# Performance work log

Hardware: AMD Instinct MI355X
Metric: run time of the kernel (lower is better)

Reference implementation:

```python
import jax, jax.numpy as jnp
import numpy as np

N = 100000   # nodes
E = 800000   # edges (avg degree ~8)
G = 64       # graphs in batch
F_IN = 64
H = 128
C = 4


def setup_inputs() -> dict:
    key = jax.random.key(0)
    ks = jax.random.split(key, 14)
    def w(k, fin, fout):
        return jax.random.normal(k, (fin, fout), dtype=jnp.float32) * (1.0 / np.sqrt(fin))
    inp = {
        "x": jax.random.normal(ks[0], (N, F_IN), dtype=jnp.float32),
        "W1": w(ks[1], F_IN, H), "b1": jnp.zeros((H,), jnp.float32),
        "W2": w(ks[2], H, H),    "b2": jnp.zeros((H,), jnp.float32),
        "W3": w(ks[3], H, H),    "b3": jnp.zeros((H,), jnp.float32),
        "fw1": w(ks[4], H, H),   "fb1": jnp.zeros((H,), jnp.float32),
        "fw2": w(ks[5], H, C),   "fb2": jnp.zeros((C,), jnp.float32),
        "edge_index": jax.random.randint(ks[6], (2, E), 0, N, dtype=jnp.int32),
        "batch": jnp.sort(jax.random.randint(ks[7], (N,), 0, G, dtype=jnp.int32)),
    }
    return inp


def gcn_conv(x, W, b, src, dst):
    """PyG GCNConv: linear transform, add self-loops, symmetric deg^-1/2 norm, scatter-add."""
    h = x @ W                                                    # [N, H]
    deg = jax.ops.segment_sum(jnp.ones((E,), x.dtype), dst, num_segments=N) + 1.0  # self-loop
    dinv = jax.lax.rsqrt(deg)                                    # [N]
    norm = dinv[src] * dinv[dst]                                 # [E]
    agg = jax.ops.segment_sum(h[src] * norm[:, None], dst, num_segments=N)
    agg = agg + h * (dinv * dinv)[:, None]                       # self-loop term (norm = 1/deg)
    return agg + b


def reference(x, W1, b1, W2, b2, W3, b3, fw1, fb1, fw2, fb2, edge_index, batch):
    src, dst = edge_index[0], edge_index[1]
    h = jax.nn.relu(gcn_conv(x, W1, b1, src, dst))
    h = jax.nn.relu(gcn_conv(h, W2, b2, src, dst))
    h = gcn_conv(h, W3, b3, src, dst)
    # global mean pool over graphs
    s = jax.ops.segment_sum(h, batch, num_segments=G)            # [G, H]
    cnt = jax.ops.segment_sum(jnp.ones((N,), h.dtype), batch, num_segments=G)
    pooled = s / jnp.maximum(cnt, 1.0)[:, None]
    z = jax.nn.relu(pooled @ fw1 + fb1)
    return z @ fw2 + fb2                                          # [G, C]
```

## Files before the change

### kernel.cpp

```cpp
#include <hip/hip_runtime.h>

#define N_NODES 100000
#define N_EDGES 800000
#define G_GRAPHS 64
#define F_INPUT 64
#define H_DIM 128
#define C_OUT 4
#define CSR_CAP 32
#define EDGE_BLOCKS (N_EDGES / 256)
#define CONV_BLOCKS ((N_NODES + 255) / 256)
#define WPACK_BLOCKS 20
#define FILL_SEG 4
#define FILL_CHUNKS 250
#define FILL_RANGE (N_NODES / FILL_SEG)
#define FILL_CHUNK (N_EDGES / FILL_CHUNKS)
#define FILL_BLOCKS (FILL_SEG * FILL_CHUNKS)
#define SEG_SPAN (FILL_RANGE * CSR_CAP)

typedef __attribute__((ext_vector_type(8))) short bf16x8;
typedef __attribute__((ext_vector_type(8))) unsigned short u16x8;
typedef __attribute__((ext_vector_type(4))) float f32x4;

__device__ inline unsigned short f2bf(float f) {
    union { float f; unsigned int u; } v; v.f = f;
    unsigned int u = v.u + 0x7FFFu + ((v.u >> 16) & 1u);
    return (unsigned short)(u >> 16);
}
__device__ inline float bf2f(unsigned short b) {
    union { unsigned int u; float f; } v; v.u = ((unsigned int)b) << 16;
    return v.f;
}
__device__ inline float2 unpack_pair(unsigned int u) {
    union { unsigned int u; float f; } a, b;
    a.u = u << 16; b.u = u & 0xFFFF0000u;
    float2 r; r.x = a.f; r.y = b.f; return r;
}
__device__ inline unsigned char f2fp8(float v) {
    int r = __builtin_amdgcn_cvt_pk_fp8_f32(v, 0.0f, 0, false);
    return (unsigned char)(r & 0xFF);
}

__device__ inline void wpack_one(const float* __restrict__ W, unsigned short* __restrict__ hi,
                                 unsigned short* __restrict__ lo, int K, int t)
{
    int lane = t & 63;
    int tile = t >> 6;
    int KS = K / 32;
    int ct = tile / KS, ks = tile % KS;
    int n  = ct * 16 + (lane & 15);
    int k0 = ks * 32 + (lane >> 4) * 8;
    #pragma unroll
    for (int j = 0; j < 8; j++) {
        float w = W[(k0 + j) * H_DIM + n];
        unsigned short h = f2bf(w);
        hi[t * 8 + j] = h;
        lo[t * 8 + j] = f2bf(w - bf2f(h));
    }
}

__global__ __launch_bounds__(256) void hist_kernel(
    const int* __restrict__ dst, int* __restrict__ cnt, int* __restrict__ paddr,
    const float* __restrict__ W1, const float* __restrict__ W2, const float* __restrict__ W3,
    unsigned short* __restrict__ w1hi, unsigned short* __restrict__ w1lo,
    unsigned short* __restrict__ w2hi, unsigned short* __restrict__ w2lo,
    unsigned short* __restrict__ w3hi, unsigned short* __restrict__ w3lo)
{
    int b = blockIdx.x;
    if (b < EDGE_BLOCKS) {
        int e = b * 256 + threadIdx.x;
        int d = dst[e];
        int sl = atomicAdd(&cnt[d], 1);
        paddr[e] = (sl < CSR_CAP) ? d * CSR_CAP + sl : -1;
        return;
    }
    b -= EDGE_BLOCKS;
    int t = b * 256 + threadIdx.x;
    if (t < 1024)       wpack_one(W1, w1hi, w1lo, F_INPUT, t);
    else if (t < 3072)  wpack_one(W2, w2hi, w2lo, H_DIM, t - 1024);
    else                wpack_one(W3, w3hi, w3lo, H_DIM, t - 3072);
}

__global__ __launch_bounds__(256) void prep_kernel(
    const int* __restrict__ paddr, const int* __restrict__ src,
    int* __restrict__ csr,
    const int* __restrict__ cnti, const float4* __restrict__ x4,
    float* __restrict__ dinv, unsigned int* __restrict__ xb_u,
    unsigned int* __restrict__ p1z, unsigned int* __restrict__ p3z)
{
    int b = blockIdx.x;
    if (b < FILL_BLOCKS) {
        const int r   = b & (FILL_SEG - 1);
        const int m   = b >> 2;
        const int plo = r * SEG_SPAN;
        const int phi = plo + SEG_SPAN;
        const int e0  = m * FILL_CHUNK;
        for (int e = e0 + threadIdx.x; e < e0 + FILL_CHUNK; e += 256) {
            int pa = paddr[e];
            if (pa >= plo && pa < phi)
                csr[pa] = src[e];
        }
        return;
    }
    b -= FILL_BLOCKS;
    __shared__ float dl[256];
    int i = b * 256 + threadIdx.x;
    float dv = 0.0f;
    if (i < N_NODES) {
        int c  = cnti[i];
        int dc = min(c, CSR_CAP);
        dv = rsqrtf((float)c + 1.0f);
        dinv[i] = dv;
        int pad = (dc + 7) & ~7;
        for (int s2 = dc; s2 < pad; s2++)
            csr[(size_t)i * CSR_CAP + s2] = N_NODES;
    } else if (i == N_NODES) {
        for (int c = 0; c < 32; c++) {
            xb_u[(size_t)N_NODES * 32 + c] = 0u;
            p1z [(size_t)N_NODES * 32 + c] = 0u;
            p3z [(size_t)N_NODES * 32 + c] = 0u;
        }
    }
    dl[threadIdx.x] = dv;
    __syncthreads();
    const int row_base = b * 256;
    for (int c = threadIdx.x; c < 256 * 16; c += 256) {
        int r = c >> 4;
        int row = row_base + r;
        if (row < N_NODES) {
            float d2 = dl[r];
            float4 v = x4[(size_t)row * 16 + (c & 15)];
            size_t o = ((size_t)row * 16 + (c & 15)) * 2;
            xb_u[o + 0] = (unsigned int)f2bf(v.x * d2) | ((unsigned int)f2bf(v.y * d2) << 16);
            xb_u[o + 1] = (unsigned int)f2bf(v.z * d2) | ((unsigned int)f2bf(v.w * d2) << 16);
        }
    }
}

__global__ __launch_bounds__(256) void gemm_g1f_kernel(
    const uint2* __restrict__ xb2, const int* __restrict__ cnti,
    const int* __restrict__ csr, const float* __restrict__ dinv,
    const unsigned short* __restrict__ whi, const unsigned short* __restrict__ wlo,
    const float* __restrict__ bias, unsigned char* __restrict__ out8)
{
    constexpr int KS = 2;
    __shared__ unsigned short As[16 * 64];
    uint2* As2 = (uint2*)As;
    const int tid  = threadIdx.x;
    const int row0 = blockIdx.x * 16;

    {
        int r  = tid >> 4;
        int f8 = tid & 15;
        int gr = row0 + r;
        int dc = min(cnti[gr], CSR_CAP);
        int beg  = gr * CSR_CAP;
        int end8 = beg + ((dc + 7) & ~7);
        const uint2* base = xb2 + f8;
        float a0, a1, a2, a3;
        {
            uint2 w = base[(size_t)gr * 16];
            float2 p0 = unpack_pair(w.x), p1 = unpack_pair(w.y);
            a0 = p0.x; a1 = p0.y; a2 = p1.x; a3 = p1.y;
        }
        for (int e = beg; e < end8; e += 8) {
            int4 c0 = *(const int4*)(csr + e);
            int4 c1 = *(const int4*)(csr + e + 4);
            uint2 w0 = base[(size_t)c0.x * 16];
            uint2 w1 = base[(size_t)c0.y * 16];
            uint2 w2 = base[(size_t)c0.z * 16];
            uint2 w3 = base[(size_t)c0.w * 16];
            uint2 w4 = base[(size_t)c1.x * 16];
            uint2 w5 = base[(size_t)c1.y * 16];
            uint2 w6 = base[(size_t)c1.z * 16];
            uint2 w7 = base[(size_t)c1.w * 16];
            #pragma unroll
            for (uint2 w : {w0, w1, w2, w3, w4, w5, w6, w7}) {
                float2 p0 = unpack_pair(w.x), p1 = unpack_pair(w.y);
                a0 += p0.x; a1 += p0.y; a2 += p1.x; a3 += p1.y;
            }
        }
        float dv = dinv[gr];
        uint2 o;
        o.x = (unsigned int)f2bf(a0 * dv) | ((unsigned int)f2bf(a1 * dv) << 16);
        o.y = (unsigned int)f2bf(a2 * dv) | ((unsigned int)f2bf(a3 * dv) << 16);
        int ks = f8 >> 3, quad = (f8 >> 1) & 3, bb = f8 & 1;
        As2[((ks * 64 + quad * 16 + r) << 1) | bb] = o;
    }
    __syncthreads();

    const int w = tid >> 6, lane = tid & 63;
    const int quad = lane >> 4, l16 = lane & 15;
    const int ct0 = w * 2;

    f32x4 acc[2];
    acc[0] = (f32x4)(0.0f);
    acc[1] = (f32x4)(0.0f);
    #pragma unroll
    for (int ks = 0; ks < KS; ks++) {
        bf16x8 a0 = *(const bf16x8*)(As + (ks * 64 + lane) * 8);
        bf16x8 bh[2], bl[2];
        #pragma unroll
        for (int c = 0; c < 2; c++) {
            bh[c] = *(const bf16x8*)(whi + ((size_t)((ct0 + c) * KS + ks) * 64 + lane) * 8);
            bl[c] = *(const bf16x8*)(wlo + ((size_t)((ct0 + c) * KS + ks) * 64 + lane) * 8);
        }
        #pragma unroll
        for (int c = 0; c < 2; c++) {
            acc[c] = __builtin_amdgcn_mfma_f32_16x16x32_bf16(a0, bh[c], acc[c], 0, 0, 0);
            acc[c] = __builtin_amdgcn_mfma_f32_16x16x32_bf16(a0, bl[c], acc[c], 0, 0, 0);
        }
    }
    float bv[2];
    #pragma unroll
    for (int c = 0; c < 2; c++) bv[c] = bias[(ct0 + c) * 16 + l16];
    #pragma unroll
    for (int reg = 0; reg < 4; reg++) {
        int row = row0 + quad * 4 + reg;
        #pragma unroll
        for (int c = 0; c < 2; c++) {
            float val = fmaxf(acc[c][reg] + bv[c], 0.0f);
            out8[(size_t)row * H_DIM + (ct0 + c) * 16 + l16] = f2fp8(val);
        }
    }
}

__device__ inline void acc_u2(uint2 w, float* __restrict__ a) {
    auto l0 = __builtin_amdgcn_cvt_pk_f32_fp8(w.x, false);
    auto h0 = __builtin_amdgcn_cvt_pk_f32_fp8(w.x, true);
    auto l1 = __builtin_amdgcn_cvt_pk_f32_fp8(w.y, false);
    auto h1 = __builtin_amdgcn_cvt_pk_f32_fp8(w.y, true);
    a[0] += l0[0]; a[1] += l0[1]; a[2] += h0[0]; a[3] += h0[1];
    a[4] += l1[0]; a[5] += l1[1]; a[6] += h1[0]; a[7] += h1[1];
}
__device__ inline void gather_fp8_u2(
    const uint2* __restrict__ base, const int* __restrict__ csr,
    int i, int beg, int end8, float* __restrict__ a)
{
    acc_u2(base[(size_t)i * 16], a);
    for (int e = beg; e < end8; e += 8) {
        int4 c0 = *(const int4*)(csr + e);
        int4 c1 = *(const int4*)(csr + e + 4);
        uint2 w0 = base[(size_t)c0.x * 16];
        uint2 w1 = base[(size_t)c0.y * 16];
        uint2 w2 = base[(size_t)c0.z * 16];
        uint2 w3 = base[(size_t)c0.w * 16];
        uint2 w4 = base[(size_t)c1.x * 16];
        uint2 w5 = base[(size_t)c1.y * 16];
        uint2 w6 = base[(size_t)c1.z * 16];
        uint2 w7 = base[(size_t)c1.w * 16];
        acc_u2(w0, a); acc_u2(w1, a); acc_u2(w2, a); acc_u2(w3, a);
        acc_u2(w4, a); acc_u2(w5, a); acc_u2(w6, a); acc_u2(w7, a);
    }
}

__global__ __launch_bounds__(256) void gemm_g2f_kernel(
    const uint2* __restrict__ hs8, const int* __restrict__ cnti,
    const int* __restrict__ csr, const float* __restrict__ dinv,
    const unsigned short* __restrict__ whi, const unsigned short* __restrict__ wlo,
    const float* __restrict__ bias, unsigned char* __restrict__ out8)
{
    constexpr int KS = 4;
    __shared__ unsigned short As[16 * 128];
    uint4* As4 = (uint4*)As;
    const int tid  = threadIdx.x;
    const int row0 = blockIdx.x * 16;

    {
        int r  = tid >> 4;
        int f8 = tid & 15;
        int gr = row0 + r;
        int dc = min(cnti[gr], CSR_CAP);
        int beg  = gr * CSR_CAP;
        int end8 = beg + ((dc + 7) & ~7);
        float a[8] = {0, 0, 0, 0, 0, 0, 0, 0};
        gather_fp8_u2(hs8 + f8, csr, gr, beg, end8, a);
        float dv = dinv[gr];
        float4 b0 = *(const float4*)(bias + f8 * 8);
        float4 b1 = *(const float4*)(bias + f8 * 8 + 4);
        float v0 = fmaxf(a[0] * dv + b0.x, 0.0f);
        float v1 = fmaxf(a[1] * dv + b0.y, 0.0f);
        float v2 = fmaxf(a[2] * dv + b0.z, 0.0f);
        float v3 = fmaxf(a[3] * dv + b0.w, 0.0f);
        float v4 = fmaxf(a[4] * dv + b1.x, 0.0f);
        float v5 = fmaxf(a[5] * dv + b1.y, 0.0f);
        float v6 = fmaxf(a[6] * dv + b1.z, 0.0f);
        float v7 = fmaxf(a[7] * dv + b1.w, 0.0f);
        uint4 o;
        o.x = (unsigned int)f2bf(v0) | ((unsigned int)f2bf(v1) << 16);
        o.y = (unsigned int)f2bf(v2) | ((unsigned int)f2bf(v3) << 16);
        o.z = (unsigned int)f2bf(v4) | ((unsigned int)f2bf(v5) << 16);
        o.w = (unsigned int)f2bf(v6) | ((unsigned int)f2bf(v7) << 16);
        As4[(f8 >> 2) * 64 + (f8 & 3) * 16 + r] = o;
    }
    __syncthreads();

    const int w = tid >> 6, lane = tid & 63;
    const int quad = lane >> 4, l16 = lane & 15;
    const int ct0 = w * 2;

    f32x4 acc[2];
    acc[0] = (f32x4)(0.0f);
    acc[1] = (f32x4)(0.0f);
    #pragma unroll
    for (int ks = 0; ks < KS; ks++) {
        bf16x8 a0 = *(const bf16x8*)(As + (ks * 64 + lane) * 8);
        bf16x8 bh[2], bl[2];
        #pragma unroll
        for (int c = 0; c < 2; c++) {
            bh[c] = *(const bf16x8*)(whi + ((size_t)((ct0 + c) * KS + ks) * 64 + lane) * 8);
            bl[c] = *(const bf16x8*)(wlo + ((size_t)((ct0 + c) * KS + ks) * 64 + lane) * 8);
        }
        #pragma unroll
        for (int c = 0; c < 2; c++) {
            acc[c] = __builtin_amdgcn_mfma_f32_16x16x32_bf16(a0, bh[c], acc[c], 0, 0, 0);
            acc[c] = __builtin_amdgcn_mfma_f32_16x16x32_bf16(a0, bl[c], acc[c], 0, 0, 0);
        }
    }
    #pragma unroll
    for (int reg = 0; reg < 4; reg++) {
        int row = row0 + quad * 4 + reg;
        float dvr = dinv[row];
        #pragma unroll
        for (int c = 0; c < 2; c++)
            out8[(size_t)row * H_DIM + (ct0 + c) * 16 + l16] = f2fp8(acc[c][reg] * dvr);
    }
}

__global__ __launch_bounds__(256) void gather3_kernel(
    const uint2* __restrict__ hs8, const int* __restrict__ cnti,
    const int* __restrict__ csr, const float* __restrict__ dinv,
    const float* __restrict__ bias, uint4* __restrict__ outb)
{
    int idx = blockIdx.x * 256 + threadIdx.x;
    int i  = idx >> 4;
    int f8 = idx & 15;
    int dc = min(cnti[i], CSR_CAP);
    int beg  = i * CSR_CAP;
    int end8 = beg + ((dc + 7) & ~7);
    float a[8] = {0, 0, 0, 0, 0, 0, 0, 0};
    gather_fp8_u2(hs8 + f8, csr, i, beg, end8, a);
    float dv = dinv[i];
    float4 b0 = *(const float4*)(bias + f8 * 8);
    float4 b1 = *(const float4*)(bias + f8 * 8 + 4);
    uint4 o;
    o.x = (unsigned int)f2bf(a[0] * dv + b0.x) | ((unsigned int)f2bf(a[1] * dv + b0.y) << 16);
    o.y = (unsigned int)f2bf(a[2] * dv + b0.z) | ((unsigned int)f2bf(a[3] * dv + b0.w) << 16);
    o.z = (unsigned int)f2bf(a[4] * dv + b1.x) | ((unsigned int)f2bf(a[5] * dv + b1.y) << 16);
    o.w = (unsigned int)f2bf(a[6] * dv + b1.z) | ((unsigned int)f2bf(a[7] * dv + b1.w) << 16);
    outb[(size_t)i * 16 + f8] = o;
}

template <int K, bool BIAS_RELU, bool IN_FP8>
__global__ __launch_bounds__(256) void mfma_gemm_kernel(
    const void* __restrict__ inv, const unsigned short* __restrict__ whi,
    const unsigned short* __restrict__ wlo, const float* __restrict__ dinv,
    const float* __restrict__ bias, unsigned char* __restrict__ out8)
{
    constexpr int KS = K / 32;
    __shared__ unsigned short As[128 * K];

    const int tid  = threadIdx.x;
    const int row0 = blockIdx.x * 128;

    const int CH = 128 * K / 8;
    for (int c = tid; c < CH; c += 256) {
        int mt   = c / (KS * 64);
        int rest = c % (KS * 64);
        int ks   = rest / 64;
        int ln   = rest % 64;
        int r    = mt * 16 + (ln & 15);
        int k    = ks * 32 + (ln >> 4) * 8;
        int gr   = row0 + r; if (gr >= N_NODES) gr = N_NODES - 1;
        if constexpr (IN_FP8) {
            const unsigned char* in8 = (const unsigned char*)inv;
            uint2 t = *(const uint2*)(in8 + (size_t)gr * K + k);
            auto f0 = __builtin_amdgcn_cvt_pk_f32_fp8(t.x, false);
            auto f1 = __builtin_amdgcn_cvt_pk_f32_fp8(t.x, true);
            auto f2 = __builtin_amdgcn_cvt_pk_f32_fp8(t.y, false);
            auto f3 = __builtin_amdgcn_cvt_pk_f32_fp8(t.y, true);
            unsigned int* Au = (unsigned int*)(As + c * 8);
            Au[0] = (unsigned int)f2bf(f0[0]) | ((unsigned int)f2bf(f0[1]) << 16);
            Au[1] = (unsigned int)f2bf(f1[0]) | ((unsigned int)f2bf(f1[1]) << 16);
            Au[2] = (unsigned int)f2bf(f2[0]) | ((unsigned int)f2bf(f2[1]) << 16);
            Au[3] = (unsigned int)f2bf(f3[0]) | ((unsigned int)f2bf(f3[1]) << 16);
        } else {
            const unsigned short* in16 = (const unsigned short*)inv;
            *(u16x8*)(As + c * 8) = *(const u16x8*)(in16 + (size_t)gr * K + k);
        }
    }
    __syncthreads();

    const int w = tid >> 6, lane = tid & 63;
    const int quad = lane >> 4, l16 = lane & 15;

    f32x4 acc[2][8];
    #pragma unroll
    for (int rt = 0; rt < 2; rt++)
        #pragma unroll
        for (int ct = 0; ct < 8; ct++) acc[rt][ct] = (f32x4)(0.0f);

    #pragma unroll
    for (int ks = 0; ks < KS; ks++) {
        bf16x8 a0 = *(const bf16x8*)(As + (((w * 2 + 0) * KS + ks) * 64 + lane) * 8);
        bf16x8 a1 = *(const bf16x8*)(As + (((w * 2 + 1) * KS + ks) * 64 + lane) * 8);
        bf16x8 bh[8], bl[8];
        #pragma unroll
        for (int ct = 0; ct < 8; ct++) {
            bh[ct] = *(const bf16x8*)(whi + ((size_t)(ct * KS + ks) * 64 + lane) * 8);
            bl[ct] = *(const bf16x8*)(wlo + ((size_t)(ct * KS + ks) * 64 + lane) * 8);
        }
        #pragma unroll
        for (int ct = 0; ct < 8; ct++) {
            acc[0][ct] = __builtin_amdgcn_mfma_f32_16x16x32_bf16(a0, bh[ct], acc[0][ct], 0, 0, 0);
            acc[0][ct] = __builtin_amdgcn_mfma_f32_16x16x32_bf16(a0, bl[ct], acc[0][ct], 0, 0, 0);
            acc[1][ct] = __builtin_amdgcn_mfma_f32_16x16x32_bf16(a1, bh[ct], acc[1][ct], 0, 0, 0);
            acc[1][ct] = __builtin_amdgcn_mfma_f32_16x16x32_bf16(a1, bl[ct], acc[1][ct], 0, 0, 0);
        }
    }

    float bv[8];
    if (BIAS_RELU) {
        #pragma unroll
        for (int ct = 0; ct < 8; ct++) bv[ct] = bias[ct * 16 + l16];
    }

    #pragma unroll
    for (int rt = 0; rt < 2; rt++) {
        #pragma unroll
        for (int reg = 0; reg < 4; reg++) {
            int row = row0 + w * 32 + rt * 16 + quad * 4 + reg;
            if (row < N_NODES) {
                float dv = BIAS_RELU ? 0.0f : dinv[row];
                #pragma unroll
                for (int ct = 0; ct < 8; ct++) {
                    float val;
                    if (BIAS_RELU) val = fmaxf(acc[rt][ct][reg] + bv[ct], 0.0f);
                    else           val = acc[rt][ct][reg] * dv;
                    out8[(size_t)row * H_DIM + ct * 16 + l16] = f2fp8(val);
                }
            }
        }
    }
}

__global__ __launch_bounds__(128) void pool_kernel(
    const unsigned short* __restrict__ A, const int* __restrict__ batch,
    float* __restrict__ s, float* __restrict__ cnt)
{
    const int RPB = 32;
    int row0 = blockIdx.x * RPB;
    int f = threadIdx.x;
    int g0 = batch[row0];
    int g1 = batch[row0 + RPB - 1];
    if (g0 == g1) {
        float acc = 0.0f;
        #pragma unroll
        for (int r = 0; r < RPB; r++)
            acc += bf2f(A[(size_t)(row0 + r) * H_DIM + f]);
        unsafeAtomicAdd(&s[g0 * H_DIM + f], acc);
        if (f == 0) unsafeAtomicAdd(&cnt[g0], (float)RPB);
    } else {
        float acc = 0.0f;
        int cur = g0, c = 0;
        for (int r = 0; r < RPB; r++) {
            int g = batch[row0 + r];
            if (g != cur) {
                unsafeAtomicAdd(&s[cur * H_DIM + f], acc);
                if (f == 0) unsafeAtomicAdd(&cnt[cur], (float)c);
                cur = g; acc = 0.0f; c = 0;
            }
            acc += bf2f(A[(size_t)(row0 + r) * H_DIM + f]);
            c++;
        }
        unsafeAtomicAdd(&s[cur * H_DIM + f], acc);
        if (f == 0) unsafeAtomicAdd(&cnt[cur], (float)c);
    }
}

__global__ __launch_bounds__(128) void mlp_kernel(
    const float* __restrict__ s, const float* __restrict__ cnt,
    const float* __restrict__ fw1, const float* __restrict__ fb1,
    const float* __restrict__ fw2, const float* __restrict__ fb2,
    float* __restrict__ out)
{
    __shared__ float p[H_DIM];
    __shared__ float z[H_DIM];
    int g = blockIdx.x;
    int f = threadIdx.x;
    float c = fmaxf(cnt[g], 1.0f);
    p[f] = s[g * H_DIM + f] / c;
    __syncthreads();
    float acc = fb1[f];
    for (int k = 0; k < H_DIM; k++) acc = fmaf(p[k], fw1[k * H_DIM + f], acc);
    z[f] = fmaxf(acc, 0.0f);
    __syncthreads();
    if (f < C_OUT) {
        float o = fb2[f];
        for (int k = 0; k < H_DIM; k++) o = fmaf(z[k], fw2[k * C_OUT + f], o);
        out[g * C_OUT + f] = o;
    }
}

extern "C" void kernel_launch(void* const* d_in, const int* in_sizes, int n_in,
                              void* d_out, int out_size, void* d_ws, size_t ws_size,
                              hipStream_t stream)
{
    const float* x   = (const float*)d_in[0];
    const float* W1  = (const float*)d_in[1];
    const float* b1  = (const float*)d_in[2];
    const float* W2  = (const float*)d_in[3];
    const float* b2  = (const float*)d_in[4];
    const float* W3  = (const float*)d_in[5];
    const float* b3  = (const float*)d_in[6];
    const float* fw1 = (const float*)d_in[7];
    const float* fb1 = (const float*)d_in[8];
    const float* fw2 = (const float*)d_in[9];
    const float* fb2 = (const float*)d_in[10];
    const int*   ei  = (const int*)d_in[11];
    const int*   bat = (const int*)d_in[12];
    const int* esrc = ei;
    const int* edst = ei + N_EDGES;
    float* out = (float*)d_out;

    char* ws = (char*)d_ws;
    unsigned short* xb   = (unsigned short*)ws; ws += (size_t)(N_NODES + 1) * F_INPUT * 2;
    unsigned short* aggB = (unsigned short*)ws; ws += (size_t)N_NODES * H_DIM * 2;
    unsigned char*  p0 = (unsigned char*)ws;  ws += (size_t)(N_NODES + 1) * H_DIM;
    unsigned char*  p1 = (unsigned char*)ws;  ws += (size_t)(N_NODES + 1) * H_DIM;
    unsigned char*  p3 = (unsigned char*)ws;  ws += (size_t)(N_NODES + 1) * H_DIM;
    unsigned short* w1hi = (unsigned short*)ws; ws += H_DIM * F_INPUT * 2;
    unsigned short* w1lo = (unsigned short*)ws; ws += H_DIM * F_INPUT * 2;
    unsigned short* w2hi = (unsigned short*)ws; ws += H_DIM * H_DIM * 2;
    unsigned short* w2lo = (unsigned short*)ws; ws += H_DIM * H_DIM * 2;
    unsigned short* w3hi = (unsigned short*)ws; ws += H_DIM * H_DIM * 2;
    unsigned short* w3lo = (unsigned short*)ws; ws += H_DIM * H_DIM * 2;
    float* dinv = (float*)ws;  ws += N_NODES * 4;
    int* paddr  = (int*)ws;    ws += (size_t)N_EDGES * 4;
    int* csr    = (int*)ws;    ws += (size_t)N_NODES * CSR_CAP * 4;
    int*   cnti = (int*)ws;    ws += N_NODES * 4;
    float* s    = (float*)ws;  ws += G_GRAPHS * H_DIM * 4;
    float* cnt  = (float*)ws;  ws += G_GRAPHS * 4;

    hipMemsetAsync(cnti, 0, (N_NODES + G_GRAPHS * H_DIM + G_GRAPHS) * sizeof(int), stream);

    hist_kernel<<<EDGE_BLOCKS + WPACK_BLOCKS, 256, 0, stream>>>(
        edst, cnti, paddr, W1, W2, W3, w1hi, w1lo, w2hi, w2lo, w3hi, w3lo);
    prep_kernel<<<FILL_BLOCKS + CONV_BLOCKS, 256, 0, stream>>>(
        paddr, esrc, csr, cnti, (const float4*)x, dinv, (unsigned int*)xb,
        (unsigned int*)p1, (unsigned int*)p3);

    const int gemm_grid = (N_NODES + 127) / 128;

    gemm_g1f_kernel<<<N_NODES / 16, 256, 0, stream>>>(
        (const uint2*)xb, cnti, csr, dinv, w1hi, w1lo, b1, p0);
    mfma_gemm_kernel<128, false, true><<<gemm_grid, 256, 0, stream>>>(
        p0, w2hi, w2lo, dinv, nullptr, p1);
    gemm_g2f_kernel<<<N_NODES / 16, 256, 0, stream>>>(
        (const uint2*)p1, cnti, csr, dinv, w3hi, w3lo, b2, p3);
    gather3_kernel<<<(N_NODES * 16) / 256, 256, 0, stream>>>(
        (const uint2*)p3, cnti, csr, dinv, b3, (uint4*)aggB);

    pool_kernel<<<N_NODES / 32, 128, 0, stream>>>(aggB, bat, s, cnt);
    mlp_kernel<<<G_GRAPHS, 128, 0, stream>>>(s, cnt, fw1, fb1, fw2, fb2, out);
}
```

Baseline: 288.0 us.

## Reorder GCN layers as aggregate-then-transform and fuse gather into GEMM kernels

Layers 2 and 3 now aggregate the raw previous-layer features, scaling each neighbour by its own dinv, and then apply the weight matrix, instead of transforming first and aggregating afterwards. This uses (A·X)·W = A·(X·W) to merge the standalone 128-row GEMM and the separate gather3 kernel into two fused gather+MFMA kernels, which drops one full-node-array write and read and one launch. In exchange each gathered edge now does an extra dinv lookup, and the quantisation points move, which can change numerical error.

```diff
diff --git a/kernel.cpp b/kernel.cpp
--- a/kernel.cpp
+++ b/kernel.cpp
@@ -85,7 +85,7 @@
     int* __restrict__ csr,
     const int* __restrict__ cnti, const float4* __restrict__ x4,
     float* __restrict__ dinv, unsigned int* __restrict__ xb_u,
-    unsigned int* __restrict__ p1z, unsigned int* __restrict__ p3z)
+    unsigned int* __restrict__ p0z, unsigned int* __restrict__ h2z)
 {
     int b = blockIdx.x;
     if (b < FILL_BLOCKS) {
@@ -114,10 +114,11 @@
         for (int s2 = dc; s2 < pad; s2++)
             csr[(size_t)i * CSR_CAP + s2] = N_NODES;
     } else if (i == N_NODES) {
+        dinv[N_NODES] = 0.0f;
         for (int c = 0; c < 32; c++) {
             xb_u[(size_t)N_NODES * 32 + c] = 0u;
-            p1z [(size_t)N_NODES * 32 + c] = 0u;
-            p3z [(size_t)N_NODES * 32 + c] = 0u;
+            p0z [(size_t)N_NODES * 32 + c] = 0u;
+            h2z [(size_t)N_NODES * 32 + c] = 0u;
         }
     }
     dl[threadIdx.x] = dv;
@@ -224,22 +225,26 @@
     }
 }
 
-__device__ inline void acc_u2(uint2 w, float* __restrict__ a) {
+__device__ inline void accw(uint2 w, float sc, float* __restrict__ a) {
     auto l0 = __builtin_amdgcn_cvt_pk_f32_fp8(w.x, false);
     auto h0 = __builtin_amdgcn_cvt_pk_f32_fp8(w.x, true);
     auto l1 = __builtin_amdgcn_cvt_pk_f32_fp8(w.y, false);
     auto h1 = __builtin_amdgcn_cvt_pk_f32_fp8(w.y, true);
-    a[0] += l0[0]; a[1] += l0[1]; a[2] += h0[0]; a[3] += h0[1];
-    a[4] += l1[0]; a[5] += l1[1]; a[6] += h1[0]; a[7] += h1[1];
-}
-__device__ inline void gather_fp8_u2(
+    a[0] = fmaf(sc, l0[0], a[0]); a[1] = fmaf(sc, l0[1], a[1]);
+    a[2] = fmaf(sc, h0[0], a[2]); a[3] = fmaf(sc, h0[1], a[3]);
+    a[4] = fmaf(sc, l1[0], a[4]); a[5] = fmaf(sc, l1[1], a[5]);
+    a[6] = fmaf(sc, h1[0], a[6]); a[7] = fmaf(sc, h1[1], a[7]);
+}
+__device__ inline void gather_fp8_w(
     const uint2* __restrict__ base, const int* __restrict__ csr,
-    int i, int beg, int end8, float* __restrict__ a)
-{
-    acc_u2(base[(size_t)i * 16], a);
+    const float* __restrict__ dinv, int i, int beg, int end8, float* __restrict__ a)
+{
+    accw(base[(size_t)i * 16], dinv[i], a);
     for (int e = beg; e < end8; e += 8) {
         int4 c0 = *(const int4*)(csr + e);
         int4 c1 = *(const int4*)(csr + e + 4);
+        float s0 = dinv[c0.x], s1 = dinv[c0.y], s2 = dinv[c0.z], s3 = dinv[c0.w];
+        float s4 = dinv[c1.x], s5 = dinv[c1.y], s6 = dinv[c1.z], s7 = dinv[c1.w];
         uint2 w0 = base[(size_t)c0.x * 16];
         uint2 w1 = base[(size_t)c0.y * 16];
         uint2 w2 = base[(size_t)c0.z * 16];
@@ -248,16 +253,17 @@
         uint2 w5 = base[(size_t)c1.y * 16];
         uint2 w6 = base[(size_t)c1.z * 16];
         uint2 w7 = base[(size_t)c1.w * 16];
-        acc_u2(w0, a); acc_u2(w1, a); acc_u2(w2, a); acc_u2(w3, a);
-        acc_u2(w4, a); acc_u2(w5, a); acc_u2(w6, a); acc_u2(w7, a);
-    }
-}
-
-__global__ __launch_bounds__(256) void gemm_g2f_kernel(
+        accw(w0, s0, a); accw(w1, s1, a); accw(w2, s2, a); accw(w3, s3, a);
+        accw(w4, s4, a); accw(w5, s5, a); accw(w6, s6, a); accw(w7, s7, a);
+    }
+}
+
+template <bool RELU_FP8>
+__global__ __launch_bounds__(256) void wgemm_kernel(
     const uint2* __restrict__ hs8, const int* __restrict__ cnti,
     const int* __restrict__ csr, const float* __restrict__ dinv,
     const unsigned short* __restrict__ whi, const unsigned short* __restrict__ wlo,
-    const float* __restrict__ bias, unsigned char* __restrict__ out8)
+    const float* __restrict__ bias, void* __restrict__ outv)
 {
     constexpr int KS = 4;
     __shared__ unsigned short As[16 * 128];
@@ -273,23 +279,12 @@
         int beg  = gr * CSR_CAP;
         int end8 = beg + ((dc + 7) & ~7);
         float a[8] = {0, 0, 0, 0, 0, 0, 0, 0};
-        gather_fp8_u2(hs8 + f8, csr, gr, beg, end8, a);
-        float dv = dinv[gr];
-        float4 b0 = *(const float4*)(bias + f8 * 8);
-        float4 b1 = *(const float4*)(bias + f8 * 8 + 4);
-        float v0 = fmaxf(a[0] * dv + b0.x, 0.0f);
-        float v1 = fmaxf(a[1] * dv + b0.y, 0.0f);
-        float v2 = fmaxf(a[2] * dv + b0.z, 0.0f);
-        float v3 = fmaxf(a[3] * dv + b0.w, 0.0f);
-        float v4 = fmaxf(a[4] * dv + b1.x, 0.0f);
-        float v5 = fmaxf(a[5] * dv + b1.y, 0.0f);
-        float v6 = fmaxf(a[6] * dv + b1.z, 0.0f);
-        float v7 = fmaxf(a[7] * dv + b1.w, 0.0f);
+        gather_fp8_w(hs8 + f8, csr, dinv, gr, beg, end8, a);
         uint4 o;
-        o.x = (unsigned int)f2bf(v0) | ((unsigned int)f2bf(v1) << 16);
-        o.y = (unsigned int)f2bf(v2) | ((unsigned int)f2bf(v3) << 16);
-        o.z = (unsigned int)f2bf(v4) | ((unsigned int)f2bf(v5) << 16);
-        o.w = (unsigned int)f2bf(v6) | ((unsigned int)f2bf(v7) << 16);
+        o.x = (unsigned int)f2bf(a[0]) | ((unsigned int)f2bf(a[1]) << 16);
+        o.y = (unsigned int)f2bf(a[2]) | ((unsigned int)f2bf(a[3]) << 16);
+        o.z = (unsigned int)f2bf(a[4]) | ((unsigned int)f2bf(a[5]) << 16);
+        o.w = (unsigned int)f2bf(a[6]) | ((unsigned int)f2bf(a[7]) << 16);
         As4[(f8 >> 2) * 64 + (f8 & 3) * 16 + r] = o;
     }
     __syncthreads();
@@ -316,128 +311,22 @@
             acc[c] = __builtin_amdgcn_mfma_f32_16x16x32_bf16(a0, bl[c], acc[c], 0, 0, 0);
         }
     }
+    float bv[2];
+    #pragma unroll
+    for (int c = 0; c < 2; c++) bv[c] = bias[(ct0 + c) * 16 + l16];
     #pragma unroll
     for (int reg = 0; reg < 4; reg++) {
         int row = row0 + quad * 4 + reg;
         float dvr = dinv[row];
         #pragma unroll
-        for (int c = 0; c < 2; c++)
-            out8[(size_t)row * H_DIM + (ct0 + c) * 16 + l16] = f2fp8(acc[c][reg] * dvr);
-    }
-}
-
-__global__ __launch_bounds__(256) void gather3_kernel(
-    const uint2* __restrict__ hs8, const int* __restrict__ cnti,
-    const int* __restrict__ csr, const float* __restrict__ dinv,
-    const float* __restrict__ bias, uint4* __restrict__ outb)
-{
-    int idx = blockIdx.x * 256 + threadIdx.x;
-    int i  = idx >> 4;
-    int f8 = idx & 15;
-    int dc = min(cnti[i], CSR_CAP);
-    int beg  = i * CSR_CAP;
-    int end8 = beg + ((dc + 7) & ~7);
-    float a[8] = {0, 0, 0, 0, 0, 0, 0, 0};
-    gather_fp8_u2(hs8 + f8, csr, i, beg, end8, a);
-    float dv = dinv[i];
-    float4 b0 = *(const float4*)(bias + f8 * 8);
-    float4 b1 = *(const float4*)(bias + f8 * 8 + 4);
-    uint4 o;
-    o.x = (unsigned int)f2bf(a[0] * dv + b0.x) | ((unsigned int)f2bf(a[1] * dv + b0.y) << 16);
-    o.y = (unsigned int)f2bf(a[2] * dv + b0.z) | ((unsigned int)f2bf(a[3] * dv + b0.w) << 16);
-    o.z = (unsigned int)f2bf(a[4] * dv + b1.x) | ((unsigned int)f2bf(a[5] * dv + b1.y) << 16);
-    o.w = (unsigned int)f2bf(a[6] * dv + b1.z) | ((unsigned int)f2bf(a[7] * dv + b1.w) << 16);
-    outb[(size_t)i * 16 + f8] = o;
-}
-
-template <int K, bool BIAS_RELU, bool IN_FP8>
-__global__ __launch_bounds__(256) void mfma_gemm_kernel(
-    const void* __restrict__ inv, const unsigned short* __restrict__ whi,
-    const unsigned short* __restrict__ wlo, const float* __restrict__ dinv,
-    const float* __restrict__ bias, unsigned char* __restrict__ out8)
-{
-    constexpr int KS = K / 32;
-    __shared__ unsigned short As[128 * K];
-
-    const int tid  = threadIdx.x;
-    const int row0 = blockIdx.x * 128;
-
-    const int CH = 128 * K / 8;
-    for (int c = tid; c < CH; c += 256) {
-        int mt   = c / (KS * 64);
-        int rest = c % (KS * 64);
-        int ks   = rest / 64;
-        int ln   = rest % 64;
-        int r    = mt * 16 + (ln & 15);
-        int k    = ks * 32 + (ln >> 4) * 8;
-        int gr   = row0 + r; if (gr >= N_NODES) gr = N_NODES - 1;
-        if constexpr (IN_FP8) {
-            const unsigned char* in8 = (const unsigned char*)inv;
-            uint2 t = *(const uint2*)(in8 + (size_t)gr * K + k);
-            auto f0 = __builtin_amdgcn_cvt_pk_f32_fp8(t.x, false);
-            auto f1 = __builtin_amdgcn_cvt_pk_f32_fp8(t.x, true);
-            auto f2 = __builtin_amdgcn_cvt_pk_f32_fp8(t.y, false);
-            auto f3 = __builtin_amdgcn_cvt_pk_f32_fp8(t.y, true);
-            unsigned int* Au = (unsigned int*)(As + c * 8);
-            Au[0] = (unsigned int)f2bf(f0[0]) | ((unsigned int)f2bf(f0[1]) << 16);
-            Au[1] = (unsigned int)f2bf(f1[0]) | ((unsigned int)f2bf(f1[1]) << 16);
-            Au[2] = (unsigned int)f2bf(f2[0]) | ((unsigned int)f2bf(f2[1]) << 16);
-            Au[3] = (unsigned int)f2bf(f3[0]) | ((unsigned int)f2bf(f3[1]) << 16);
-        } else {
-            const unsigned short* in16 = (const unsigned short*)inv;
-            *(u16x8*)(As + c * 8) = *(const u16x8*)(in16 + (size_t)gr * K + k);
-        }
-    }
-    __syncthreads();
-
-    const int w = tid >> 6, lane = tid & 63;
-    const int quad = lane >> 4, l16 = lane & 15;
-
-    f32x4 acc[2][8];
-    #pragma unroll
-    for (int rt = 0; rt < 2; rt++)
-        #pragma unroll
-        for (int ct = 0; ct < 8; ct++) acc[rt][ct] = (f32x4)(0.0f);
-
-    #pragma unroll
-    for (int ks = 0; ks < KS; ks++) {
-        bf16x8 a0 = *(const bf16x8*)(As + (((w * 2 + 0) * KS + ks) * 64 + lane) * 8);
-        bf16x8 a1 = *(const bf16x8*)(As + (((w * 2 + 1) * KS + ks) * 64 + lane) * 8);
-        bf16x8 bh[8], bl[8];
-        #pragma unroll
-        for (int ct = 0; ct < 8; ct++) {
-            bh[ct] = *(const bf16x8*)(whi + ((size_t)(ct * KS + ks) * 64 + lane) * 8);
-            bl[ct] = *(const bf16x8*)(wlo + ((size_t)(ct * KS + ks) * 64 + lane) * 8);
-        }
-        #pragma unroll
-        for (int ct = 0; ct < 8; ct++) {
-            acc[0][ct] = __builtin_amdgcn_mfma_f32_16x16x32_bf16(a0, bh[ct], acc[0][ct], 0, 0, 0);
-            acc[0][ct] = __builtin_amdgcn_mfma_f32_16x16x32_bf16(a0, bl[ct], acc[0][ct], 0, 0, 0);
-            acc[1][ct] = __builtin_amdgcn_mfma_f32_16x16x32_bf16(a1, bh[ct], acc[1][ct], 0, 0, 0);
-            acc[1][ct] = __builtin_amdgcn_mfma_f32_16x16x32_bf16(a1, bl[ct], acc[1][ct], 0, 0, 0);
-        }
-    }
-
-    float bv[8];
-    if (BIAS_RELU) {
-        #pragma unroll
-        for (int ct = 0; ct < 8; ct++) bv[ct] = bias[ct * 16 + l16];
-    }
-
-    #pragma unroll
-    for (int rt = 0; rt < 2; rt++) {
-        #pragma unroll
-        for (int reg = 0; reg < 4; reg++) {
-            int row = row0 + w * 32 + rt * 16 + quad * 4 + reg;
-            if (row < N_NODES) {
-                float dv = BIAS_RELU ? 0.0f : dinv[row];
-                #pragma unroll
-                for (int ct = 0; ct < 8; ct++) {
-                    float val;
-                    if (BIAS_RELU) val = fmaxf(acc[rt][ct][reg] + bv[ct], 0.0f);
-                    else           val = acc[rt][ct][reg] * dv;
-                    out8[(size_t)row * H_DIM + ct * 16 + l16] = f2fp8(val);
-                }
+        for (int c = 0; c < 2; c++) {
+            float val = acc[c][reg] * dvr + bv[c];
+            if constexpr (RELU_FP8) {
+                ((unsigned char*)outv)[(size_t)row * H_DIM + (ct0 + c) * 16 + l16] =
+                    f2fp8(fmaxf(val, 0.0f));
+            } else {
+                ((unsigned short*)outv)[(size_t)row * H_DIM + (ct0 + c) * 16 + l16] =
+                    f2bf(val);
             }
         }
     }
@@ -523,18 +412,17 @@
     float* out = (float*)d_out;
 
     char* ws = (char*)d_ws;
-    unsigned short* xb   = (unsigned short*)ws; ws += (size_t)(N_NODES + 1) * F_INPUT * 2;
+    unsigned short* xb = (unsigned short*)ws; ws += (size_t)(N_NODES + 1) * F_INPUT * 2;
+    unsigned char*  p0 = (unsigned char*)ws;  ws += (size_t)(N_NODES + 1) * H_DIM;
+    unsigned char*  h2 = (unsigned char*)ws;  ws += (size_t)(N_NODES + 1) * H_DIM;
     unsigned short* aggB = (unsigned short*)ws; ws += (size_t)N_NODES * H_DIM * 2;
-    unsigned char*  p0 = (unsigned char*)ws;  ws += (size_t)(N_NODES + 1) * H_DIM;
-    unsigned char*  p1 = (unsigned char*)ws;  ws += (size_t)(N_NODES + 1) * H_DIM;
-    unsigned char*  p3 = (unsigned char*)ws;  ws += (size_t)(N_NODES + 1) * H_DIM;
     unsigned short* w1hi = (unsigned short*)ws; ws += H_DIM * F_INPUT * 2;
     unsigned short* w1lo = (unsigned short*)ws; ws += H_DIM * F_INPUT * 2;
     unsigned short* w2hi = (unsigned short*)ws; ws += H_DIM * H_DIM * 2;
     unsigned short* w2lo = (unsigned short*)ws; ws += H_DIM * H_DIM * 2;
     unsigned short* w3hi = (unsigned short*)ws; ws += H_DIM * H_DIM * 2;
     unsigned short* w3lo = (unsigned short*)ws; ws += H_DIM * H_DIM * 2;
-    float* dinv = (float*)ws;  ws += N_NODES * 4;
+    float* dinv = (float*)ws;  ws += (N_NODES + 1) * 4;
     int* paddr  = (int*)ws;    ws += (size_t)N_EDGES * 4;
     int* csr    = (int*)ws;    ws += (size_t)N_NODES * CSR_CAP * 4;
     int*   cnti = (int*)ws;    ws += N_NODES * 4;
@@ -547,18 +435,14 @@
         edst, cnti, paddr, W1, W2, W3, w1hi, w1lo, w2hi, w2lo, w3hi, w3lo);
     prep_kernel<<<FILL_BLOCKS + CONV_BLOCKS, 256, 0, stream>>>(
         paddr, esrc, csr, cnti, (const float4*)x, dinv, (unsigned int*)xb,
-        (unsigned int*)p1, (unsigned int*)p3);
-
-    const int gemm_grid = (N_NODES + 127) / 128;
+        (unsigned int*)p0, (unsigned int*)h2);
 
     gemm_g1f_kernel<<<N_NODES / 16, 256, 0, stream>>>(
         (const uint2*)xb, cnti, csr, dinv, w1hi, w1lo, b1, p0);
-    mfma_gemm_kernel<128, false, true><<<gemm_grid, 256, 0, stream>>>(
-        p0, w2hi, w2lo, dinv, nullptr, p1);
-    gemm_g2f_kernel<<<N_NODES / 16, 256, 0, stream>>>(
-        (const uint2*)p1, cnti, csr, dinv, w3hi, w3lo, b2, p3);
-    gather3_kernel<<<(N_NODES * 16) / 256, 256, 0, stream>>>(
-        (const uint2*)p3, cnti, csr, dinv, b3, (uint4*)aggB);
+    wgemm_kernel<true><<<N_NODES / 16, 256, 0, stream>>>(
+        (const uint2*)p0, cnti, csr, dinv, w2hi, w2lo, b2, h2);
+    wgemm_kernel<false><<<N_NODES / 16, 256, 0, stream>>>(
+        (const uint2*)h2, cnti, csr, dinv, w3hi, w3lo, b3, aggB);
 
     pool_kernel<<<N_NODES / 32, 128, 0, stream>>>(aggB, bat, s, cnt);
     mlp_kernel<<<G_GRAPHS, 128, 0, stream>>>(s, cnt, fw1, fb1, fw2, fb2, out);
```

New measurement: 293.0 us. Within noise of the previous version (+1.8%).
